# Kernel tuning notes

Hardware: AMD Instinct MI355X
Metric: run time of the kernel (lower is better)

## Reference

```python
import jax, jax.numpy as jnp
import numpy as np

NUM_NODE = 50000
NUM_EDGE = 1_600_000
NUM_REL = 512
DIM = 64


def setup_inputs() -> dict:
    key = jax.random.key(0)
    k1, k2, k3, k4, k5, k6 = jax.random.split(key, 6)
    inp = jax.random.normal(k1, (NUM_NODE, DIM), dtype=jnp.float32)
    boundary = jax.random.normal(k2, (NUM_NODE, DIM), dtype=jnp.float32)
    node_in = jax.random.randint(k3, (NUM_EDGE,), 0, NUM_NODE)
    node_out = jax.random.randint(k4, (NUM_EDGE,), 0, NUM_NODE)
    rel = jax.random.randint(k5, (NUM_EDGE,), 0, NUM_REL)
    edge_list = jnp.stack([node_in, node_out, rel], axis=1).astype(jnp.int32)
    edge_weight = jnp.ones((NUM_EDGE,), dtype=jnp.float32)
    relation_weight = jax.random.normal(k6, (NUM_REL, DIM), dtype=jnp.float32)
    W = jax.random.normal(jax.random.fold_in(key, 7), (DIM, DIM), dtype=jnp.float32) / np.sqrt(DIM)
    b = jnp.zeros((DIM,), dtype=jnp.float32)
    return {"input": inp, "boundary": boundary, "edge_list": edge_list,
            "edge_weight": edge_weight, "relation_weight": relation_weight,
            "W": W, "b": b}


def reference(input, boundary, edge_list, edge_weight, relation_weight, W, b):
    node_in = edge_list[:, 0]
    node_out = edge_list[:, 1]
    rel = edge_list[:, 2]
    # message: DistMult = x_src * r_e   [E, D]
    msg = input[node_in] * relation_weight[rel]
    msg = msg * edge_weight[:, None]
    # std aggregation: sum and sq_sum scatters, boundary acts as an extra self-message
    s = jax.ops.segment_sum(msg, node_out, num_segments=NUM_NODE) + boundary
    sq = jax.ops.segment_sum(msg * msg, node_out, num_segments=NUM_NODE) + boundary * boundary
    deg = jax.ops.segment_sum(jnp.ones_like(edge_weight), node_out, num_segments=NUM_NODE)
    deg1 = (deg + 1.0)[:, None]  # degree_out + 1 (boundary counted)
    update = jnp.sqrt(jnp.clip(sq / deg1 - (s / deg1) ** 2, 1e-6))
    # add_model: single Linear (MLP with num_mlp_layer=1, no trailing activation)
    return update @ W.T + b
```

## Files before the change

kernel.cpp:

```cpp
#include <hip/hip_runtime.h>
#include <hip/hip_bf16.h>
#include <hip/hip_fp16.h>

#define NN  50000
#define NE  1600000
#define DIM 64
#define NBK 391

#define OFF_FLAGS  0
#define OFF_BOFF   8
#define OFF_BCUR   400
#define OFF_ROWPTR 792
#define OFF_INP16  50800
#define OFF_RELW16 1650800
#define OFF_EIDX_H 1667184

#define CHUNK 2048
#define SBCAP 8192

typedef __bf16 bf16x8 __attribute__((ext_vector_type(8)));
typedef __bf16 bf16x4 __attribute__((ext_vector_type(4)));
typedef float  f32x4  __attribute__((ext_vector_type(4)));

__device__ __forceinline__ float loadF(const void* p, int i, int bf) {
  if (bf) return __bfloat162float(((const __hip_bfloat16*)p)[i]);
  return ((const float*)p)[i];
}

__device__ __forceinline__ float4 loadF4(const void* p, int i4, int bf) {
  if (bf) {
    ushort4 u = ((const ushort4*)p)[i4];
    float4 f;
    union { unsigned int ui; float fl; } c;
    c.ui = (unsigned int)u.x << 16; f.x = c.fl;
    c.ui = (unsigned int)u.y << 16; f.y = c.fl;
    c.ui = (unsigned int)u.z << 16; f.z = c.fl;
    c.ui = (unsigned int)u.w << 16; f.w = c.fl;
    return f;
  }
  return ((const float4*)p)[i4];
}

__device__ __forceinline__ float4 h4f(ushort4 u) {
  float4 f;
  f.x = __half2float(__ushort_as_half(u.x));
  f.y = __half2float(__ushort_as_half(u.y));
  f.z = __half2float(__ushort_as_half(u.z));
  f.w = __half2float(__ushort_as_half(u.w));
  return f;
}

__device__ __forceinline__ void accum(ushort4 ua, ushort4 ur,
                                      float4& s4, float4& q4) {
  float4 a = h4f(ua), r = h4f(ur);
  float tx = a.x * r.x, ty = a.y * r.y, tz = a.z * r.z, tw = a.w * r.w;
  s4.x += tx; q4.x = fmaf(tx, tx, q4.x);
  s4.y += ty; q4.y = fmaf(ty, ty, q4.y);
  s4.z += tz; q4.z = fmaf(tz, tz, q4.z);
  s4.w += tw; q4.w = fmaf(tw, tw, q4.w);
}

__global__ void k_detect(const void* input, const void* boundary,
                         const void* relw, const void* W, const void* ew,
                         int* flags, int* boff) {
  __shared__ int cnt;
  int t = threadIdx.x;
  const void* arrs[4] = {input, boundary, relw, W};
  for (int a = 0; a < 4; ++a) {
    if (t == 0) cnt = 0;
    __syncthreads();
    const unsigned short* u = (const unsigned short*)arrs[a];
    unsigned ex = (u[2 * t] >> 7) & 0xFF;
    if (ex >= 100 && ex <= 140) atomicAdd(&cnt, 1);
    __syncthreads();
    if (t == 0) flags[a] = (cnt >= 32) ? 1 : 0;
    __syncthreads();
  }
  if (t == 0) {
    flags[4] = (((const unsigned short*)ew)[0] == 0x3F80) ? 1 : 0;
    flags[5] = 1;
  }
  for (int i = t; i < 392; i += 64) boff[i] = 0;
}

__global__ __launch_bounds__(256) void k_stage(const void* __restrict__ in,
                                               const void* __restrict__ rw,
                                               unsigned short* __restrict__ inph,
                                               unsigned short* __restrict__ rwh,
                                               const int* __restrict__ flags) {
  if (flags[0] || flags[2]) return;
  int i = blockIdx.x * 256 + threadIdx.x;
  if (i < NN * 16) {
    float4 v = ((const float4*)in)[i];
    ushort4 h;
    h.x = __half_as_ushort(__float2half(v.x));
    h.y = __half_as_ushort(__float2half(v.y));
    h.z = __half_as_ushort(__float2half(v.z));
    h.w = __half_as_ushort(__float2half(v.w));
    ((ushort4*)inph)[i] = h;
  }
  if (i < 512 * 16) {
    float4 v = ((const float4*)rw)[i];
    ushort4 h;
    h.x = __half_as_ushort(__float2half(v.x));
    h.y = __half_as_ushort(__float2half(v.y));
    h.z = __half_as_ushort(__float2half(v.z));
    h.w = __half_as_ushort(__float2half(v.w));
    ((ushort4*)rwh)[i] = h;
  }
}

__global__ __launch_bounds__(256) void k_bhist(const int* __restrict__ el,
                                               const void* __restrict__ ew,
                                               int* __restrict__ bcnt,
                                               int* __restrict__ flags) {
  __shared__ int lc[NBK];
  int t = threadIdx.x;
  int bfE = flags[4];
  for (int i = t; i < NBK; i += 256) lc[i] = 0;
  __syncthreads();
  int c0 = blockIdx.x * 8192;
  int bad = 0;
  for (int i = t; i < 8192; i += 256) {
    int e = c0 + i;
    if (e < NE) {
      atomicAdd(&lc[el[e * 3 + 1] >> 7], 1);
      if (loadF(ew, e, bfE) != 1.0f) bad = 1;
    }
  }
  if (bad) flags[5] = 0;
  __syncthreads();
  for (int i = t; i < NBK; i += 256)
    if (lc[i]) atomicAdd(&bcnt[i], lc[i]);
}

__global__ __launch_bounds__(256) void k_scanb(int* __restrict__ boff,
                                               int* __restrict__ bcur,
                                               int* __restrict__ rowptr) {
  __shared__ int sc[256];
  int t = threadIdx.x;
  int i0 = 2 * t, i1 = 2 * t + 1;
  int a = (i0 < 392) ? boff[i0] : 0;
  int b = (i1 < 392) ? boff[i1] : 0;
  sc[t] = a + b;
  __syncthreads();
  for (int off = 1; off < 256; off <<= 1) {
    int v = (t >= off) ? sc[t - off] : 0;
    __syncthreads();
    sc[t] += v;
    __syncthreads();
  }
  int excl = sc[t] - (a + b);
  if (i0 < 392) boff[i0] = excl;
  if (i1 < 392) boff[i1] = excl + a;
  if (i0 < NBK) bcur[i0] = excl;
  if (i1 < NBK) bcur[i1] = excl + a;
  if (t == 255) rowptr[NN] = sc[255];
}

__global__ __launch_bounds__(256) void k_parta(
    const int* __restrict__ el, int* __restrict__ bcur,
    int* __restrict__ eidx, const int* __restrict__ flags,
    const int* __restrict__ boff, int gb0, int gb1, int cap) {
  __shared__ int stage[CHUNK];
  __shared__ unsigned short sbk[CHUNK];
  __shared__ int lh[NBK], lbase[NBK], lh2[NBK], gbs[NBK];
  __shared__ int sc[256];
  __shared__ int total;
  int t = threadIdx.x;
  int nb = gb1 - gb0;
  int c0 = blockIdx.x * CHUNK;
  int ones = flags[5];
  int base0 = boff[gb0];
  for (int i = t; i < nb; i += 256) { lh[i] = 0; lh2[i] = 0; }
  __syncthreads();
  for (int i = t; i < CHUNK; i += 256) {
    int e = c0 + i;
    if (e < NE) {
      int b = (el[e * 3 + 1] >> 7) - gb0;
      if (b >= 0 && b < nb) atomicAdd(&lh[b], 1);
    }
  }
  __syncthreads();
  int a0 = (2 * t < nb) ? lh[2 * t] : 0;
  int a1 = (2 * t + 1 < nb) ? lh[2 * t + 1] : 0;
  sc[t] = a0 + a1;
  __syncthreads();
  for (int off = 1; off < 256; off <<= 1) {
    int v = (t >= off) ? sc[t - off] : 0;
    __syncthreads();
    sc[t] += v;
    __syncthreads();
  }
  int excl = sc[t] - (a0 + a1);
  if (2 * t < nb) {
    lbase[2 * t] = excl;
    if (a0 > 0) gbs[2 * t] = atomicAdd(&bcur[gb0 + 2 * t], a0);
  }
  if (2 * t + 1 < nb) {
    lbase[2 * t + 1] = excl + a0;
    if (a1 > 0) gbs[2 * t + 1] = atomicAdd(&bcur[gb0 + 2 * t + 1], a1);
  }
  if (t == 255) total = sc[255];
  __syncthreads();
  for (int i = t; i < CHUNK; i += 256) {
    int e = c0 + i;
    if (e < NE) {
      int nout = el[e * 3 + 1];
      int b = (nout >> 7) - gb0;
      if (b >= 0 && b < nb) {
        int r = atomicAdd(&lh2[b], 1);
        int slot = lbase[b] + r;
        int rec = ones ? (el[e * 3] | (el[e * 3 + 2] << 16) |
                          ((nout & 127) << 25))
                       : (e | ((nout & 127) << 25));
        stage[slot] = rec;
        sbk[slot] = (unsigned short)b;
      }
    }
  }
  __syncthreads();
  int tot = total;
  for (int i = t; i < tot; i += 256) {
    int b = sbk[i];
    int dst = gbs[b] + (i - lbase[b]) - base0;
    if (dst >= 0 && dst < cap) eidx[dst] = stage[i];
  }
}

__global__ __launch_bounds__(256) void k_partb(
    int* __restrict__ eidx, const int* __restrict__ boff,
    int* __restrict__ rowptr, const int* __restrict__ el,
    const int* __restrict__ flags, int gb0, int cap) {
  __shared__ int ld[SBCAP];
  __shared__ int lcnt[128], lexc[128];
  int t = threadIdx.x;
  int b = gb0 + blockIdx.x;
  int n0 = b * 128;
  int ncnt = min(128, NN - n0);
  int base0 = boff[gb0];
  int rbase = boff[b], rend = boff[b + 1];
  int cnt = rend - rbase;
  int fast = (cnt <= SBCAP) && (rend - base0 <= cap);
  if (t < 128) lcnt[t] = 0;
  __syncthreads();
  if (fast) {
    for (int i = t; i < cnt; i += 256) ld[i] = eidx[rbase - base0 + i];
    __syncthreads();
    for (int i = t; i < cnt; i += 256)
      atomicAdd(&lcnt[(((unsigned)ld[i]) >> 25) & 127], 1);
  } else {
    int lim = n0 + ncnt;
    for (int e = t; e < NE; e += 256) {
      int nout = el[e * 3 + 1];
      if (nout >= n0 && nout < lim) atomicAdd(&lcnt[nout - n0], 1);
    }
  }
  __syncthreads();
  if (t < 128) lexc[t] = lcnt[t];
  __syncthreads();
  for (int off = 1; off < 128; off <<= 1) {
    int v = 0;
    if (t < 128 && t >= off) v = lexc[t - off];
    __syncthreads();
    if (t < 128) lexc[t] += v;
    __syncthreads();
  }
  if (t < 128) lexc[t] -= lcnt[t];
  __syncthreads();
  if (t < ncnt) rowptr[n0 + t] = rbase + lexc[t];
  if (t == 0) rowptr[n0 + ncnt] = rend;
  if (t < 128) lcnt[t] = 0;
  __syncthreads();
  if (fast) {
    for (int i = t; i < cnt; i += 256) {
      int rec = ld[i];
      int l = (((unsigned)rec) >> 25) & 127;
      int r = atomicAdd(&lcnt[l], 1);
      int dst = rbase + lexc[l] + r - base0;
      if (dst >= 0 && dst < cap) eidx[dst] = rec & 0x1FFFFFF;
    }
  } else {
    int ones = flags[5];
    int lim = n0 + ncnt;
    for (int e = t; e < NE; e += 256) {
      int nout = el[e * 3 + 1];
      if (nout >= n0 && nout < lim) {
        int l = nout - n0;
        int r = atomicAdd(&lcnt[l], 1);
        int dst = rbase + lexc[l] + r - base0;
        int rec = ones ? (el[e * 3] | (el[e * 3 + 2] << 16)) : e;
        if (dst >= 0 && dst < cap) eidx[dst] = rec;
      }
    }
  }
}

__global__ __launch_bounds__(256, 4) void k_node(
    const void* __restrict__ input, const void* __restrict__ boundary,
    const int* __restrict__ el, const void* __restrict__ ew,
    const void* __restrict__ relw, const void* __restrict__ W,
    const void* __restrict__ bv, const int* __restrict__ rowptr,
    const int* __restrict__ eidx, const int* __restrict__ flags,
    const unsigned short* __restrict__ inph,
    const unsigned short* __restrict__ rwh,
    void* __restrict__ out, int lo, int hi, int cap) {
  __shared__ __bf16 updb[16][72];

  int bfI = flags[0], bfB = flags[1], bfR = flags[2], bfW = flags[3],
      bfE = flags[4], ones = flags[5];
  int t  = threadIdx.x;
  int wv = t >> 6, ln = t & 63;
  int g  = ln >> 4;
  int k  = ln & 15;
  int q  = ln >> 4;
  int n0 = lo + blockIdx.x * 16;
  int base0 = rowptr[lo];

  int cc = wv * 16 + (ln & 15);
  bf16x8 bfr0, bfr1;
  #pragma unroll
  for (int j = 0; j < 8; ++j) {
    bfr0[j] = (__bf16)loadF(W, cc * 64 + q * 8 + j, bfW);
    bfr1[j] = (__bf16)loadF(W, cc * 64 + 32 + q * 8 + j, bfW);
  }
  float bias = loadF(bv, cc, bfW);

  const ushort4* ih4 = (const ushort4*)inph;
  const ushort4* rh4 = (const ushort4*)rwh;
  int hot = (!bfI && !bfR && ones) ? 1 : 0;
  int hotH = hot && (inph != 0);

  for (int rr = 0; rr < 4; ++rr) {
    int row = wv * 4 + rr;
    int n = n0 + row;
    if (n >= hi) {
      updb[row][ln] = (__bf16)0.0f;
      continue;
    }
    int start = rowptr[n] - base0, end = rowptr[n + 1] - base0;
    int deg = end - start;
    float4 s4 = {0.f,0.f,0.f,0.f}, q4 = {0.f,0.f,0.f,0.f};
    if (hotH) {
      for (int base = start; base < end; base += 64) {
        int mm = end - base; if (mm > 64) mm = 64;
        int rec = 0;
        int idx2 = base + ln;
        if (ln < mm && idx2 < cap) rec = eidx[idx2];
        int jq = mm >> 2;
        int jmax = (mm + 3) >> 2;
        int j = 0;
        for (; j + 4 <= jq; j += 4) {
          int pk0 = __shfl(rec, j * 4 + g);
          int pk1 = __shfl(rec, j * 4 + 4 + g);
          int pk2 = __shfl(rec, j * 4 + 8 + g);
          int pk3 = __shfl(rec, j * 4 + 12 + g);
          ushort4 a0 = ih4[(pk0 & 0xFFFF) * 16 + k];
          ushort4 r0 = rh4[((pk0 >> 16) & 0x1FF) * 16 + k];
          ushort4 a1 = ih4[(pk1 & 0xFFFF) * 16 + k];
          ushort4 r1 = rh4[((pk1 >> 16) & 0x1FF) * 16 + k];
          ushort4 a2 = ih4[(pk2 & 0xFFFF) * 16 + k];
          ushort4 r2 = rh4[((pk2 >> 16) & 0x1FF) * 16 + k];
          ushort4 a3 = ih4[(pk3 & 0xFFFF) * 16 + k];
          ushort4 r3 = rh4[((pk3 >> 16) & 0x1FF) * 16 + k];
          accum(a0, r0, s4, q4);
          accum(a1, r1, s4, q4);
          accum(a2, r2, s4, q4);
          accum(a3, r3, s4, q4);
        }
        for (; j < jq; ++j) {
          int pk = __shfl(rec, j * 4 + g);
          ushort4 a = ih4[(pk & 0xFFFF) * 16 + k];
          ushort4 r = rh4[((pk >> 16) & 0x1FF) * 16 + k];
          accum(a, r, s4, q4);
        }
        for (; j < jmax; ++j) {
          int slot = j * 4 + g;
          int pk = __shfl(rec, slot & 63);
          float wsel = (slot < mm) ? 1.0f : 0.0f;
          ushort4 ua = ih4[(pk & 0xFFFF) * 16 + k];
          ushort4 ur = rh4[((pk >> 16) & 0x1FF) * 16 + k];
          float4 a = h4f(ua), r = h4f(ur);
          float tx = a.x*r.x, ty = a.y*r.y, tz = a.z*r.z, tw = a.w*r.w;
          s4.x = fmaf(wsel, tx, s4.x); q4.x = fmaf(wsel*tx, tx, q4.x);
          s4.y = fmaf(wsel, ty, s4.y); q4.y = fmaf(wsel*ty, ty, q4.y);
          s4.z = fmaf(wsel, tz, s4.z); q4.z = fmaf(wsel*tz, tz, q4.z);
          s4.w = fmaf(wsel, tw, s4.w); q4.w = fmaf(wsel*tw, tw, q4.w);
        }
      }
    } else {
      for (int base = start; base < end; base += 64) {
        int mm = end - base; if (mm > 64) mm = 64;
        int rec = 0; float wrec = 0.0f;
        int idx2 = base + ln;
        if (ln < mm && idx2 < cap) {
          rec = eidx[idx2] & 0x1FFFFFF;
          if (!ones) wrec = loadF(ew, rec, bfE);
        }
        int jmax = (mm + 3) >> 2;
        for (int j = 0; j < jmax; ++j) {
          int slot = j * 4 + g;
          int rj = __shfl(rec, slot);
          int nin, rl; float wj;
          if (ones) { nin = rj & 0xFFFF; rl = (rj >> 16) & 0x1FF; wj = 1.0f; }
          else      { nin = el[rj * 3]; rl = el[rj * 3 + 2];
                      wj = __shfl(wrec, slot); }
          float wsel = (slot < mm) ? wj : 0.0f;
          float4 a = loadF4(input, nin * 16 + k, bfI);
          float4 r = loadF4(relw, rl * 16 + k, bfR);
          float tx = a.x*r.x, ty = a.y*r.y, tz = a.z*r.z, tw = a.w*r.w;
          s4.x = fmaf(wsel, tx, s4.x); q4.x = fmaf(wsel*tx, tx, q4.x);
          s4.y = fmaf(wsel, ty, s4.y); q4.y = fmaf(wsel*ty, ty, q4.y);
          s4.z = fmaf(wsel, tz, s4.z); q4.z = fmaf(wsel*tz, tz, q4.z);
          s4.w = fmaf(wsel, tw, s4.w); q4.w = fmaf(wsel*tw, tw, q4.w);
        }
      }
    }
    s4.x += __shfl_xor(s4.x, 16); s4.x += __shfl_xor(s4.x, 32);
    s4.y += __shfl_xor(s4.y, 16); s4.y += __shfl_xor(s4.y, 32);
    s4.z += __shfl_xor(s4.z, 16); s4.z += __shfl_xor(s4.z, 32);
    s4.w += __shfl_xor(s4.w, 16); s4.w += __shfl_xor(s4.w, 32);
    q4.x += __shfl_xor(q4.x, 16); q4.x += __shfl_xor(q4.x, 32);
    q4.y += __shfl_xor(q4.y, 16); q4.y += __shfl_xor(q4.y, 32);
    q4.z += __shfl_xor(q4.z, 16); q4.z += __shfl_xor(q4.z, 32);
    q4.w += __shfl_xor(q4.w, 16); q4.w += __shfl_xor(q4.w, 32);
    if (g == 0) {
      float4 b4 = loadF4(boundary, n * 16 + k, bfB);
      float dg = (float)deg + 1.0f;
      float sv, qv;
      bf16x4 u;
      sv = (s4.x + b4.x) / dg; qv = (q4.x + b4.x * b4.x) / dg;
      u[0] = (__bf16)sqrtf(fmaxf(qv - sv * sv, 1e-6f));
      sv = (s4.y + b4.y) / dg; qv = (q4.y + b4.y * b4.y) / dg;
      u[1] = (__bf16)sqrtf(fmaxf(qv - sv * sv, 1e-6f));
      sv = (s4.z + b4.z) / dg; qv = (q4.z + b4.z * b4.z) / dg;
      u[2] = (__bf16)sqrtf(fmaxf(qv - sv * sv, 1e-6f));
      sv = (s4.w + b4.w) / dg; qv = (q4.w + b4.w * b4.w) / dg;
      u[3] = (__bf16)sqrtf(fmaxf(qv - sv * sv, 1e-6f));
      *(bf16x4*)&updb[row][4 * k] = u;
    }
  }
  __syncthreads();

  bf16x8 af0 = *(const bf16x8*)&updb[ln & 15][q * 8];
  bf16x8 af1 = *(const bf16x8*)&updb[ln & 15][32 + q * 8];
  f32x4 acc = {0.f, 0.f, 0.f, 0.f};
  acc = __builtin_amdgcn_mfma_f32_16x16x32_bf16(af0, bfr0, acc, 0, 0, 0);
  acc = __builtin_amdgcn_mfma_f32_16x16x32_bf16(af1, bfr1, acc, 0, 0, 0);
  #pragma unroll
  for (int i = 0; i < 4; ++i) {
    int n = n0 + q * 4 + i;
    if (n < hi) {
      float v = acc[i] + bias;
      if (bfI) ((__hip_bfloat16*)out)[n * 64 + cc] = __float2bfloat16(v);
      else     ((float*)out)[n * 64 + cc] = v;
    }
  }
}

extern "C" void kernel_launch(void* const* d_in, const int* in_sizes, int n_in,
                              void* d_out, int out_size, void* d_ws, size_t ws_size,
                              hipStream_t stream) {
  const void* input    = d_in[0];
  const void* boundary = d_in[1];
  const int*  edges    = (const int*)d_in[2];
  const void* eweight  = d_in[3];
  const void* relw     = d_in[4];
  const void* W        = d_in[5];
  const void* bv       = d_in[6];

  int* wsI    = (int*)d_ws;
  int* flags  = wsI + OFF_FLAGS;
  int* boff   = wsI + OFF_BOFF;
  int* bcur   = wsI + OFF_BCUR;
  int* rowptr = wsI + OFF_ROWPTR;

  long avail = (long)(ws_size / 4) - OFF_INP16;
  int useH = (avail >= (long)NE + 1600000 + 16384) ? 1 : 0;
  unsigned short* inph = useH ? (unsigned short*)(wsI + OFF_INP16) : 0;
  unsigned short* rwh  = useH ? (unsigned short*)(wsI + OFF_RELW16) : 0;
  int* eidx = useH ? (wsI + OFF_EIDX_H) : (wsI + OFF_INP16);
  long cap = useH ? (avail - 1600000 - 16384) : avail;
  if (cap < 1) cap = 1;
  int npass;
  if      (cap >= (long)NE) npass = 1;
  else if (cap >= 1000000)  npass = 2;
  else if (cap >= 520000)   npass = 4;
  else                      npass = 8;

  k_detect<<<1, 64, 0, stream>>>(input, boundary, relw, W, eweight,
                                 flags, boff);
  if (useH)
    k_stage<<<(NN * 16 + 255) / 256, 256, 0, stream>>>(input, relw, inph,
                                                       rwh, flags);
  k_bhist<<<(NE + 8191) / 8192, 256, 0, stream>>>(edges, eweight, boff, flags);
  k_scanb<<<1, 256, 0, stream>>>(boff, bcur, rowptr);

  const int PA_NB = (NE + CHUNK - 1) / CHUNK;
  for (int p = 0; p < npass; ++p) {
    int gb0 = NBK * p / npass;
    int gb1 = NBK * (p + 1) / npass;
    int lo = gb0 * 128;
    int hi = (gb1 * 128 < NN) ? gb1 * 128 : NN;
    k_parta<<<PA_NB, 256, 0, stream>>>(edges, bcur, eidx, flags, boff,
                                       gb0, gb1, (int)cap);
    k_partb<<<gb1 - gb0, 256, 0, stream>>>(eidx, boff, rowptr, edges, flags,
                                           gb0, (int)cap);
    k_node<<<(hi - lo + 15) / 16, 256, 0, stream>>>(
        input, boundary, edges, eweight, relw, W, bv, rowptr, eidx, flags,
        inph, rwh, d_out, lo, hi, (int)cap);
  }
}
```

Before: 259.5 us.

## Cache relation weights in LDS with 1024-thread node blocks

k_node now runs 1024-thread blocks covering 64 nodes and copies the whole bf16 relation-weight table (64 KB) into shared memory, so the per-edge relation gathers become LDS reads instead of global loads. The updb staging buffer now reuses that shared array: the table is dead by then and results wait in registers across an extra barrier. The W fragment load is moved after aggregation and mapped per wave to a column quarter. It also doubles the edge-partition CHUNK. The 64 KB of LDS per block limits occupancy, and each block pays a table fill.

After: 251.9 us. 2.9% less time.

```diff
diff --git a/kernel.cpp b/kernel.cpp
--- a/kernel.cpp
+++ b/kernel.cpp
@@ -15,7 +15,7 @@
 #define OFF_RELW16 1650800
 #define OFF_EIDX_H 1667184
 
-#define CHUNK 2048
+#define CHUNK 4096
 #define SBCAP 8192
 
 typedef __bf16 bf16x8 __attribute__((ext_vector_type(8)));
@@ -296,7 +296,7 @@
   }
 }
 
-__global__ __launch_bounds__(256, 4) void k_node(
+__global__ __launch_bounds__(1024, 8) void k_node(
     const void* __restrict__ input, const void* __restrict__ boundary,
     const int* __restrict__ el, const void* __restrict__ ew,
     const void* __restrict__ relw, const void* __restrict__ W,
@@ -305,7 +305,8 @@
     const unsigned short* __restrict__ inph,
     const unsigned short* __restrict__ rwh,
     void* __restrict__ out, int lo, int hi, int cap) {
-  __shared__ __bf16 updb[16][72];
+  __shared__ ushort4 smraw[8192];
+  __bf16 (*updb)[72] = reinterpret_cast<__bf16(*)[72]>(smraw);
 
   int bfI = flags[0], bfB = flags[1], bfR = flags[2], bfW = flags[3],
       bfE = flags[4], ones = flags[5];
@@ -314,30 +315,30 @@
   int g  = ln >> 4;
   int k  = ln & 15;
   int q  = ln >> 4;
-  int n0 = lo + blockIdx.x * 16;
+  int n0 = lo + blockIdx.x * 64;
   int base0 = rowptr[lo];
-
-  int cc = wv * 16 + (ln & 15);
-  bf16x8 bfr0, bfr1;
-  #pragma unroll
-  for (int j = 0; j < 8; ++j) {
-    bfr0[j] = (__bf16)loadF(W, cc * 64 + q * 8 + j, bfW);
-    bfr1[j] = (__bf16)loadF(W, cc * 64 + 32 + q * 8 + j, bfW);
-  }
-  float bias = loadF(bv, cc, bfW);
+  int tt = wv >> 2, cq = wv & 3;
 
   const ushort4* ih4 = (const ushort4*)inph;
-  const ushort4* rh4 = (const ushort4*)rwh;
   int hot = (!bfI && !bfR && ones) ? 1 : 0;
   int hotH = hot && (inph != 0);
 
+  if (hotH) {
+    const ushort4* rh4g = (const ushort4*)rwh;
+    for (int i = t; i < 8192; i += 1024) smraw[i] = rh4g[i];
+  }
+  __syncthreads();
+
+  bf16x4 usv[4];
+
+  #pragma unroll
   for (int rr = 0; rr < 4; ++rr) {
     int row = wv * 4 + rr;
     int n = n0 + row;
-    if (n >= hi) {
-      updb[row][ln] = (__bf16)0.0f;
-      continue;
-    }
+    bf16x4 uz; uz[0] = (__bf16)0.f; uz[1] = (__bf16)0.f;
+    uz[2] = (__bf16)0.f; uz[3] = (__bf16)0.f;
+    usv[rr] = uz;
+    if (n >= hi) continue;
     int start = rowptr[n] - base0, end = rowptr[n + 1] - base0;
     int deg = end - start;
     float4 s4 = {0.f,0.f,0.f,0.f}, q4 = {0.f,0.f,0.f,0.f};
@@ -356,13 +357,13 @@
           int pk2 = __shfl(rec, j * 4 + 8 + g);
           int pk3 = __shfl(rec, j * 4 + 12 + g);
           ushort4 a0 = ih4[(pk0 & 0xFFFF) * 16 + k];
-          ushort4 r0 = rh4[((pk0 >> 16) & 0x1FF) * 16 + k];
           ushort4 a1 = ih4[(pk1 & 0xFFFF) * 16 + k];
-          ushort4 r1 = rh4[((pk1 >> 16) & 0x1FF) * 16 + k];
           ushort4 a2 = ih4[(pk2 & 0xFFFF) * 16 + k];
-          ushort4 r2 = rh4[((pk2 >> 16) & 0x1FF) * 16 + k];
           ushort4 a3 = ih4[(pk3 & 0xFFFF) * 16 + k];
-          ushort4 r3 = rh4[((pk3 >> 16) & 0x1FF) * 16 + k];
+          ushort4 r0 = smraw[((pk0 >> 16) & 0x1FF) * 16 + k];
+          ushort4 r1 = smraw[((pk1 >> 16) & 0x1FF) * 16 + k];
+          ushort4 r2 = smraw[((pk2 >> 16) & 0x1FF) * 16 + k];
+          ushort4 r3 = smraw[((pk3 >> 16) & 0x1FF) * 16 + k];
           accum(a0, r0, s4, q4);
           accum(a1, r1, s4, q4);
           accum(a2, r2, s4, q4);
@@ -371,7 +372,7 @@
         for (; j < jq; ++j) {
           int pk = __shfl(rec, j * 4 + g);
           ushort4 a = ih4[(pk & 0xFFFF) * 16 + k];
-          ushort4 r = rh4[((pk >> 16) & 0x1FF) * 16 + k];
+          ushort4 r = smraw[((pk >> 16) & 0x1FF) * 16 + k];
           accum(a, r, s4, q4);
         }
         for (; j < jmax; ++j) {
@@ -379,7 +380,7 @@
           int pk = __shfl(rec, slot & 63);
           float wsel = (slot < mm) ? 1.0f : 0.0f;
           ushort4 ua = ih4[(pk & 0xFFFF) * 16 + k];
-          ushort4 ur = rh4[((pk >> 16) & 0x1FF) * 16 + k];
+          ushort4 ur = smraw[((pk >> 16) & 0x1FF) * 16 + k];
           float4 a = h4f(ua), r = h4f(ur);
           float tx = a.x*r.x, ty = a.y*r.y, tz = a.z*r.z, tw = a.w*r.w;
           s4.x = fmaf(wsel, tx, s4.x); q4.x = fmaf(wsel*tx, tx, q4.x);
@@ -437,19 +438,34 @@
       u[2] = (__bf16)sqrtf(fmaxf(qv - sv * sv, 1e-6f));
       sv = (s4.w + b4.w) / dg; qv = (q4.w + b4.w * b4.w) / dg;
       u[3] = (__bf16)sqrtf(fmaxf(qv - sv * sv, 1e-6f));
-      *(bf16x4*)&updb[row][4 * k] = u;
-    }
-  }
-  __syncthreads();
-
-  bf16x8 af0 = *(const bf16x8*)&updb[ln & 15][q * 8];
-  bf16x8 af1 = *(const bf16x8*)&updb[ln & 15][32 + q * 8];
+      usv[rr] = u;
+    }
+  }
+  __syncthreads();
+  if (g == 0) {
+    #pragma unroll
+    for (int rr = 0; rr < 4; ++rr)
+      *(bf16x4*)&updb[wv * 4 + rr][4 * k] = usv[rr];
+  }
+  __syncthreads();
+
+  int cc = cq * 16 + (ln & 15);
+  bf16x8 bfr0, bfr1;
+  #pragma unroll
+  for (int j = 0; j < 8; ++j) {
+    bfr0[j] = (__bf16)loadF(W, cc * 64 + q * 8 + j, bfW);
+    bfr1[j] = (__bf16)loadF(W, cc * 64 + 32 + q * 8 + j, bfW);
+  }
+  float bias = loadF(bv, cc, bfW);
+
+  bf16x8 af0 = *(const bf16x8*)&updb[tt * 16 + (ln & 15)][q * 8];
+  bf16x8 af1 = *(const bf16x8*)&updb[tt * 16 + (ln & 15)][32 + q * 8];
   f32x4 acc = {0.f, 0.f, 0.f, 0.f};
   acc = __builtin_amdgcn_mfma_f32_16x16x32_bf16(af0, bfr0, acc, 0, 0, 0);
   acc = __builtin_amdgcn_mfma_f32_16x16x32_bf16(af1, bfr1, acc, 0, 0, 0);
   #pragma unroll
   for (int i = 0; i < 4; ++i) {
-    int n = n0 + q * 4 + i;
+    int n = n0 + tt * 16 + q * 4 + i;
     if (n < hi) {
       float v = acc[i] + bias;
       if (bfI) ((__hip_bfloat16*)out)[n * 64 + cc] = __float2bfloat16(v);
@@ -506,7 +522,7 @@
                                        gb0, gb1, (int)cap);
     k_partb<<<gb1 - gb0, 256, 0, stream>>>(eidx, boff, rowptr, edges, flags,
                                            gb0, (int)cap);
-    k_node<<<(hi - lo + 15) / 16, 256, 0, stream>>>(
+    k_node<<<(hi - lo + 63) / 64, 1024, 0, stream>>>(
         input, boundary, edges, eweight, relw, W, bv, rowptr, eidx, flags,
         inph, rwh, d_out, lo, hi, (int)cap);
   }
```

## Fuse per-bucket local sort into node kernel, keep sorted edges in LDS

Applied to the files above, without the earlier changes.

Merges the bucket-local counting sort (k_partb) into the node aggregation kernel. Each 1024-thread block now owns one 128-node bucket, sorts its edges into shared memory and reads them from LDS instead of writing and re-reading a global CSR (rowptr). This removes one kernel launch and a global round trip of the edge index array. The slow fallback becomes a per-node full edge scan, and occupancy drops to 391 blocks of 1024 threads, which lowers parallelism per pass. CHUNK in the partition kernel is also doubled.

Result: faster. 241.1 us (-7.1%).

```diff
diff --git a/kernel.cpp b/kernel.cpp
--- a/kernel.cpp
+++ b/kernel.cpp
@@ -10,13 +10,12 @@
 #define OFF_FLAGS  0
 #define OFF_BOFF   8
 #define OFF_BCUR   400
-#define OFF_ROWPTR 792
 #define OFF_INP16  50800
 #define OFF_RELW16 1650800
 #define OFF_EIDX_H 1667184
 
-#define CHUNK 2048
-#define SBCAP 8192
+#define CHUNK 4096
+#define SBCAP 7936
 
 typedef __bf16 bf16x8 __attribute__((ext_vector_type(8)));
 typedef __bf16 bf16x4 __attribute__((ext_vector_type(4)));
@@ -135,8 +134,7 @@
 }
 
 __global__ __launch_bounds__(256) void k_scanb(int* __restrict__ boff,
-                                               int* __restrict__ bcur,
-                                               int* __restrict__ rowptr) {
+                                               int* __restrict__ bcur) {
   __shared__ int sc[256];
   int t = threadIdx.x;
   int i0 = 2 * t, i1 = 2 * t + 1;
@@ -155,7 +153,6 @@
   if (i1 < 392) boff[i1] = excl + a;
   if (i0 < NBK) bcur[i0] = excl;
   if (i1 < NBK) bcur[i1] = excl + a;
-  if (t == 255) rowptr[NN] = sc[255];
 }
 
 __global__ __launch_bounds__(256) void k_parta(
@@ -228,193 +225,173 @@
   }
 }
 
-__global__ __launch_bounds__(256) void k_partb(
-    int* __restrict__ eidx, const int* __restrict__ boff,
-    int* __restrict__ rowptr, const int* __restrict__ el,
-    const int* __restrict__ flags, int gb0, int cap) {
+__global__ __launch_bounds__(1024, 8) void k_node(
+    const void* __restrict__ input, const void* __restrict__ boundary,
+    const int* __restrict__ el, const void* __restrict__ ew,
+    const void* __restrict__ relw, const void* __restrict__ W,
+    const void* __restrict__ bv, const int* __restrict__ boff,
+    const int* __restrict__ eidx, const int* __restrict__ flags,
+    const unsigned short* __restrict__ inph,
+    const unsigned short* __restrict__ rwh,
+    void* __restrict__ out, int gb0, int hi, int cap) {
   __shared__ int ld[SBCAP];
-  __shared__ int lcnt[128], lexc[128];
+  __shared__ int ld2[SBCAP];
+  __shared__ int lstart[128], lend[128], lcnt[128];
+  __bf16 (*updb)[72] = reinterpret_cast<__bf16(*)[72]>(ld);
+
+  int bfI = flags[0], bfB = flags[1], bfR = flags[2], bfW = flags[3],
+      bfE = flags[4], ones = flags[5];
   int t = threadIdx.x;
-  int b = gb0 + blockIdx.x;
-  int n0 = b * 128;
-  int ncnt = min(128, NN - n0);
+  int wv = t >> 6, ln = t & 63;
+  int g = ln >> 4;
+  int k = ln & 15;
+  int q = ln >> 4;
+  int B = gb0 + blockIdx.x;
+  int n0 = B * 128;
   int base0 = boff[gb0];
-  int rbase = boff[b], rend = boff[b + 1];
+  int rbase = boff[B], rend = boff[B + 1];
   int cnt = rend - rbase;
   int fast = (cnt <= SBCAP) && (rend - base0 <= cap);
+
   if (t < 128) lcnt[t] = 0;
   __syncthreads();
   if (fast) {
-    for (int i = t; i < cnt; i += 256) ld[i] = eidx[rbase - base0 + i];
-    __syncthreads();
-    for (int i = t; i < cnt; i += 256)
+    for (int i = t; i < cnt; i += 1024) ld[i] = eidx[rbase - base0 + i];
+    __syncthreads();
+    for (int i = t; i < cnt; i += 1024)
       atomicAdd(&lcnt[(((unsigned)ld[i]) >> 25) & 127], 1);
-  } else {
-    int lim = n0 + ncnt;
-    for (int e = t; e < NE; e += 256) {
-      int nout = el[e * 3 + 1];
-      if (nout >= n0 && nout < lim) atomicAdd(&lcnt[nout - n0], 1);
-    }
-  }
-  __syncthreads();
-  if (t < 128) lexc[t] = lcnt[t];
+  }
+  __syncthreads();
+  if (t < 128) lend[t] = lcnt[t];
   __syncthreads();
   for (int off = 1; off < 128; off <<= 1) {
     int v = 0;
-    if (t < 128 && t >= off) v = lexc[t - off];
-    __syncthreads();
-    if (t < 128) lexc[t] += v;
-    __syncthreads();
-  }
-  if (t < 128) lexc[t] -= lcnt[t];
-  __syncthreads();
-  if (t < ncnt) rowptr[n0 + t] = rbase + lexc[t];
-  if (t == 0) rowptr[n0 + ncnt] = rend;
-  if (t < 128) lcnt[t] = 0;
+    if (t < 128 && t >= off) v = lend[t - off];
+    __syncthreads();
+    if (t < 128) lend[t] += v;
+    __syncthreads();
+  }
+  if (t < 128) { lstart[t] = lend[t] - lcnt[t]; lcnt[t] = 0; }
   __syncthreads();
   if (fast) {
-    for (int i = t; i < cnt; i += 256) {
+    for (int i = t; i < cnt; i += 1024) {
       int rec = ld[i];
       int l = (((unsigned)rec) >> 25) & 127;
       int r = atomicAdd(&lcnt[l], 1);
-      int dst = rbase + lexc[l] + r - base0;
-      if (dst >= 0 && dst < cap) eidx[dst] = rec & 0x1FFFFFF;
-    }
-  } else {
-    int ones = flags[5];
-    int lim = n0 + ncnt;
-    for (int e = t; e < NE; e += 256) {
-      int nout = el[e * 3 + 1];
-      if (nout >= n0 && nout < lim) {
-        int l = nout - n0;
-        int r = atomicAdd(&lcnt[l], 1);
-        int dst = rbase + lexc[l] + r - base0;
-        int rec = ones ? (el[e * 3] | (el[e * 3 + 2] << 16)) : e;
-        if (dst >= 0 && dst < cap) eidx[dst] = rec;
-      }
-    }
-  }
-}
-
-__global__ __launch_bounds__(256, 4) void k_node(
-    const void* __restrict__ input, const void* __restrict__ boundary,
-    const int* __restrict__ el, const void* __restrict__ ew,
-    const void* __restrict__ relw, const void* __restrict__ W,
-    const void* __restrict__ bv, const int* __restrict__ rowptr,
-    const int* __restrict__ eidx, const int* __restrict__ flags,
-    const unsigned short* __restrict__ inph,
-    const unsigned short* __restrict__ rwh,
-    void* __restrict__ out, int lo, int hi, int cap) {
-  __shared__ __bf16 updb[16][72];
-
-  int bfI = flags[0], bfB = flags[1], bfR = flags[2], bfW = flags[3],
-      bfE = flags[4], ones = flags[5];
-  int t  = threadIdx.x;
-  int wv = t >> 6, ln = t & 63;
-  int g  = ln >> 4;
-  int k  = ln & 15;
-  int q  = ln >> 4;
-  int n0 = lo + blockIdx.x * 16;
-  int base0 = rowptr[lo];
-
-  int cc = wv * 16 + (ln & 15);
-  bf16x8 bfr0, bfr1;
-  #pragma unroll
-  for (int j = 0; j < 8; ++j) {
-    bfr0[j] = (__bf16)loadF(W, cc * 64 + q * 8 + j, bfW);
-    bfr1[j] = (__bf16)loadF(W, cc * 64 + 32 + q * 8 + j, bfW);
-  }
-  float bias = loadF(bv, cc, bfW);
+      ld2[lstart[l] + r] = rec;
+    }
+  }
+  __syncthreads();
 
   const ushort4* ih4 = (const ushort4*)inph;
   const ushort4* rh4 = (const ushort4*)rwh;
-  int hot = (!bfI && !bfR && ones) ? 1 : 0;
-  int hotH = hot && (inph != 0);
-
-  for (int rr = 0; rr < 4; ++rr) {
-    int row = wv * 4 + rr;
+  int hot = (!bfI && !bfR && ones && inph != 0) ? 1 : 0;
+
+  for (int rr = 0; rr < 8; ++rr) {
+    int row = wv * 8 + rr;
     int n = n0 + row;
     if (n >= hi) {
-      updb[row][ln] = (__bf16)0.0f;
+      if (g == 0) *(bf16x4*)&updb[row][4 * k] =
+          bf16x4{(__bf16)0.f, (__bf16)0.f, (__bf16)0.f, (__bf16)0.f};
       continue;
     }
-    int start = rowptr[n] - base0, end = rowptr[n + 1] - base0;
-    int deg = end - start;
     float4 s4 = {0.f,0.f,0.f,0.f}, q4 = {0.f,0.f,0.f,0.f};
-    if (hotH) {
-      for (int base = start; base < end; base += 64) {
-        int mm = end - base; if (mm > 64) mm = 64;
-        int rec = 0;
-        int idx2 = base + ln;
-        if (ln < mm && idx2 < cap) rec = eidx[idx2];
-        int jq = mm >> 2;
-        int jmax = (mm + 3) >> 2;
-        int j = 0;
-        for (; j + 4 <= jq; j += 4) {
-          int pk0 = __shfl(rec, j * 4 + g);
-          int pk1 = __shfl(rec, j * 4 + 4 + g);
-          int pk2 = __shfl(rec, j * 4 + 8 + g);
-          int pk3 = __shfl(rec, j * 4 + 12 + g);
-          ushort4 a0 = ih4[(pk0 & 0xFFFF) * 16 + k];
-          ushort4 r0 = rh4[((pk0 >> 16) & 0x1FF) * 16 + k];
-          ushort4 a1 = ih4[(pk1 & 0xFFFF) * 16 + k];
-          ushort4 r1 = rh4[((pk1 >> 16) & 0x1FF) * 16 + k];
-          ushort4 a2 = ih4[(pk2 & 0xFFFF) * 16 + k];
-          ushort4 r2 = rh4[((pk2 >> 16) & 0x1FF) * 16 + k];
-          ushort4 a3 = ih4[(pk3 & 0xFFFF) * 16 + k];
-          ushort4 r3 = rh4[((pk3 >> 16) & 0x1FF) * 16 + k];
-          accum(a0, r0, s4, q4);
-          accum(a1, r1, s4, q4);
-          accum(a2, r2, s4, q4);
-          accum(a3, r3, s4, q4);
+    float degf = 0.f;
+    if (fast) {
+      int start = lstart[row], end = lend[row];
+      degf = (float)(end - start);
+      if (hot) {
+        for (int base = start; base < end; base += 64) {
+          int mm = end - base; if (mm > 64) mm = 64;
+          int rec = 0;
+          if (ln < mm) rec = ld2[base + ln];
+          int jq = mm >> 2;
+          int jmax = (mm + 3) >> 2;
+          int j = 0;
+          for (; j + 4 <= jq; j += 4) {
+            int pk0 = __shfl(rec, j * 4 + g);
+            int pk1 = __shfl(rec, j * 4 + 4 + g);
+            int pk2 = __shfl(rec, j * 4 + 8 + g);
+            int pk3 = __shfl(rec, j * 4 + 12 + g);
+            ushort4 a0 = ih4[(pk0 & 0xFFFF) * 16 + k];
+            ushort4 r0 = rh4[((pk0 >> 16) & 0x1FF) * 16 + k];
+            ushort4 a1 = ih4[(pk1 & 0xFFFF) * 16 + k];
+            ushort4 r1 = rh4[((pk1 >> 16) & 0x1FF) * 16 + k];
+            ushort4 a2 = ih4[(pk2 & 0xFFFF) * 16 + k];
+            ushort4 r2 = rh4[((pk2 >> 16) & 0x1FF) * 16 + k];
+            ushort4 a3 = ih4[(pk3 & 0xFFFF) * 16 + k];
+            ushort4 r3 = rh4[((pk3 >> 16) & 0x1FF) * 16 + k];
+            accum(a0, r0, s4, q4);
+            accum(a1, r1, s4, q4);
+            accum(a2, r2, s4, q4);
+            accum(a3, r3, s4, q4);
+          }
+          for (; j < jq; ++j) {
+            int pk = __shfl(rec, j * 4 + g);
+            ushort4 a = ih4[(pk & 0xFFFF) * 16 + k];
+            ushort4 r = rh4[((pk >> 16) & 0x1FF) * 16 + k];
+            accum(a, r, s4, q4);
+          }
+          for (; j < jmax; ++j) {
+            int slot = j * 4 + g;
+            int pk = __shfl(rec, slot & 63);
+            float wsel = (slot < mm) ? 1.0f : 0.0f;
+            ushort4 ua = ih4[(pk & 0xFFFF) * 16 + k];
+            ushort4 ur = rh4[((pk >> 16) & 0x1FF) * 16 + k];
+            float4 a = h4f(ua), r = h4f(ur);
+            float tx = a.x*r.x, ty = a.y*r.y, tz = a.z*r.z, tw = a.w*r.w;
+            s4.x = fmaf(wsel, tx, s4.x); q4.x = fmaf(wsel*tx, tx, q4.x);
+            s4.y = fmaf(wsel, ty, s4.y); q4.y = fmaf(wsel*ty, ty, q4.y);
+            s4.z = fmaf(wsel, tz, s4.z); q4.z = fmaf(wsel*tz, tz, q4.z);
+            s4.w = fmaf(wsel, tw, s4.w); q4.w = fmaf(wsel*tw, tw, q4.w);
+          }
         }
-        for (; j < jq; ++j) {
-          int pk = __shfl(rec, j * 4 + g);
-          ushort4 a = ih4[(pk & 0xFFFF) * 16 + k];
-          ushort4 r = rh4[((pk >> 16) & 0x1FF) * 16 + k];
-          accum(a, r, s4, q4);
-        }
-        for (; j < jmax; ++j) {
-          int slot = j * 4 + g;
-          int pk = __shfl(rec, slot & 63);
-          float wsel = (slot < mm) ? 1.0f : 0.0f;
-          ushort4 ua = ih4[(pk & 0xFFFF) * 16 + k];
-          ushort4 ur = rh4[((pk >> 16) & 0x1FF) * 16 + k];
-          float4 a = h4f(ua), r = h4f(ur);
-          float tx = a.x*r.x, ty = a.y*r.y, tz = a.z*r.z, tw = a.w*r.w;
-          s4.x = fmaf(wsel, tx, s4.x); q4.x = fmaf(wsel*tx, tx, q4.x);
-          s4.y = fmaf(wsel, ty, s4.y); q4.y = fmaf(wsel*ty, ty, q4.y);
-          s4.z = fmaf(wsel, tz, s4.z); q4.z = fmaf(wsel*tz, tz, q4.z);
-          s4.w = fmaf(wsel, tw, s4.w); q4.w = fmaf(wsel*tw, tw, q4.w);
+      } else {
+        for (int base = start; base < end; base += 64) {
+          int mm = end - base; if (mm > 64) mm = 64;
+          int rec = 0; float wrec = 0.0f;
+          if (ln < mm) {
+            rec = ld2[base + ln] & 0x1FFFFFF;
+            if (!ones) wrec = loadF(ew, rec, bfE);
+          }
+          int jmax = (mm + 3) >> 2;
+          for (int j = 0; j < jmax; ++j) {
+            int slot = j * 4 + g;
+            int rj = __shfl(rec, slot);
+            int nin, rl; float wj;
+            if (ones) { nin = rj & 0xFFFF; rl = (rj >> 16) & 0x1FF; wj = 1.0f; }
+            else      { nin = el[rj * 3]; rl = el[rj * 3 + 2];
+                        wj = __shfl(wrec, slot); }
+            float wsel = (slot < mm) ? wj : 0.0f;
+            float4 a = loadF4(input, nin * 16 + k, bfI);
+            float4 r = loadF4(relw, rl * 16 + k, bfR);
+            float tx = a.x*r.x, ty = a.y*r.y, tz = a.z*r.z, tw = a.w*r.w;
+            s4.x = fmaf(wsel, tx, s4.x); q4.x = fmaf(wsel*tx, tx, q4.x);
+            s4.y = fmaf(wsel, ty, s4.y); q4.y = fmaf(wsel*ty, ty, q4.y);
+            s4.z = fmaf(wsel, tz, s4.z); q4.z = fmaf(wsel*tz, tz, q4.z);
+            s4.w = fmaf(wsel, tw, s4.w); q4.w = fmaf(wsel*tw, tw, q4.w);
+          }
         }
       }
     } else {
-      for (int base = start; base < end; base += 64) {
-        int mm = end - base; if (mm > 64) mm = 64;
-        int rec = 0; float wrec = 0.0f;
-        int idx2 = base + ln;
-        if (ln < mm && idx2 < cap) {
-          rec = eidx[idx2] & 0x1FFFFFF;
-          if (!ones) wrec = loadF(ew, rec, bfE);
-        }
-        int jmax = (mm + 3) >> 2;
-        for (int j = 0; j < jmax; ++j) {
-          int slot = j * 4 + g;
-          int rj = __shfl(rec, slot);
-          int nin, rl; float wj;
-          if (ones) { nin = rj & 0xFFFF; rl = (rj >> 16) & 0x1FF; wj = 1.0f; }
-          else      { nin = el[rj * 3]; rl = el[rj * 3 + 2];
-                      wj = __shfl(wrec, slot); }
-          float wsel = (slot < mm) ? wj : 0.0f;
-          float4 a = loadF4(input, nin * 16 + k, bfI);
-          float4 r = loadF4(relw, rl * 16 + k, bfR);
-          float tx = a.x*r.x, ty = a.y*r.y, tz = a.z*r.z, tw = a.w*r.w;
-          s4.x = fmaf(wsel, tx, s4.x); q4.x = fmaf(wsel*tx, tx, q4.x);
-          s4.y = fmaf(wsel, ty, s4.y); q4.y = fmaf(wsel*ty, ty, q4.y);
-          s4.z = fmaf(wsel, tz, s4.z); q4.z = fmaf(wsel*tz, tz, q4.z);
-          s4.w = fmaf(wsel, tw, s4.w); q4.w = fmaf(wsel*tw, tw, q4.w);
-        }
+      float degc = 0.f;
+      for (int e0 = g; e0 < NE; e0 += 4) {
+        int nout = el[e0 * 3 + 1];
+        if (nout != n) continue;
+        degc += 1.0f;
+        int nin = el[e0 * 3], rl = el[e0 * 3 + 2];
+        float wj = ones ? 1.0f : loadF(ew, e0, bfE);
+        float4 a = loadF4(input, nin * 16 + k, bfI);
+        float4 r = loadF4(relw, rl * 16 + k, bfR);
+        float tx = wj*a.x*r.x, ty = wj*a.y*r.y, tz = wj*a.z*r.z,
+              tw = wj*a.w*r.w;
+        s4.x += tx; q4.x = fmaf(tx, tx, q4.x);
+        s4.y += ty; q4.y = fmaf(ty, ty, q4.y);
+        s4.z += tz; q4.z = fmaf(tz, tz, q4.z);
+        s4.w += tw; q4.w = fmaf(tw, tw, q4.w);
       }
+      degc += __shfl_xor(degc, 16); degc += __shfl_xor(degc, 32);
+      degf = degc;
     }
     s4.x += __shfl_xor(s4.x, 16); s4.x += __shfl_xor(s4.x, 32);
     s4.y += __shfl_xor(s4.y, 16); s4.y += __shfl_xor(s4.y, 32);
@@ -426,7 +403,7 @@
     q4.w += __shfl_xor(q4.w, 16); q4.w += __shfl_xor(q4.w, 32);
     if (g == 0) {
       float4 b4 = loadF4(boundary, n * 16 + k, bfB);
-      float dg = (float)deg + 1.0f;
+      float dg = degf + 1.0f;
       float sv, qv;
       bf16x4 u;
       sv = (s4.x + b4.x) / dg; qv = (q4.x + b4.x * b4.x) / dg;
@@ -442,18 +419,30 @@
   }
   __syncthreads();
 
-  bf16x8 af0 = *(const bf16x8*)&updb[ln & 15][q * 8];
-  bf16x8 af1 = *(const bf16x8*)&updb[ln & 15][32 + q * 8];
-  f32x4 acc = {0.f, 0.f, 0.f, 0.f};
-  acc = __builtin_amdgcn_mfma_f32_16x16x32_bf16(af0, bfr0, acc, 0, 0, 0);
-  acc = __builtin_amdgcn_mfma_f32_16x16x32_bf16(af1, bfr1, acc, 0, 0, 0);
+  int tt = wv >> 1, chh = wv & 1;
+  bf16x8 af0 = *(const bf16x8*)&updb[tt * 16 + (ln & 15)][q * 8];
+  bf16x8 af1 = *(const bf16x8*)&updb[tt * 16 + (ln & 15)][32 + q * 8];
   #pragma unroll
-  for (int i = 0; i < 4; ++i) {
-    int n = n0 + q * 4 + i;
-    if (n < hi) {
-      float v = acc[i] + bias;
-      if (bfI) ((__hip_bfloat16*)out)[n * 64 + cc] = __float2bfloat16(v);
-      else     ((float*)out)[n * 64 + cc] = v;
+  for (int hh = 0; hh < 2; ++hh) {
+    int cc = chh * 32 + hh * 16 + (ln & 15);
+    bf16x8 bfr0, bfr1;
+    #pragma unroll
+    for (int j = 0; j < 8; ++j) {
+      bfr0[j] = (__bf16)loadF(W, cc * 64 + q * 8 + j, bfW);
+      bfr1[j] = (__bf16)loadF(W, cc * 64 + 32 + q * 8 + j, bfW);
+    }
+    float bias = loadF(bv, cc, bfW);
+    f32x4 accv = {0.f, 0.f, 0.f, 0.f};
+    accv = __builtin_amdgcn_mfma_f32_16x16x32_bf16(af0, bfr0, accv, 0, 0, 0);
+    accv = __builtin_amdgcn_mfma_f32_16x16x32_bf16(af1, bfr1, accv, 0, 0, 0);
+    #pragma unroll
+    for (int i = 0; i < 4; ++i) {
+      int nn = n0 + tt * 16 + q * 4 + i;
+      if (nn < hi) {
+        float v = accv[i] + bias;
+        if (bfI) ((__hip_bfloat16*)out)[nn * 64 + cc] = __float2bfloat16(v);
+        else     ((float*)out)[nn * 64 + cc] = v;
+      }
     }
   }
 }
@@ -473,7 +462,6 @@
   int* flags  = wsI + OFF_FLAGS;
   int* boff   = wsI + OFF_BOFF;
   int* bcur   = wsI + OFF_BCUR;
-  int* rowptr = wsI + OFF_ROWPTR;
 
   long avail = (long)(ws_size / 4) - OFF_INP16;
   int useH = (avail >= (long)NE + 1600000 + 16384) ? 1 : 0;
@@ -494,20 +482,17 @@
     k_stage<<<(NN * 16 + 255) / 256, 256, 0, stream>>>(input, relw, inph,
                                                        rwh, flags);
   k_bhist<<<(NE + 8191) / 8192, 256, 0, stream>>>(edges, eweight, boff, flags);
-  k_scanb<<<1, 256, 0, stream>>>(boff, bcur, rowptr);
+  k_scanb<<<1, 256, 0, stream>>>(boff, bcur);
 
   const int PA_NB = (NE + CHUNK - 1) / CHUNK;
   for (int p = 0; p < npass; ++p) {
     int gb0 = NBK * p / npass;
     int gb1 = NBK * (p + 1) / npass;
-    int lo = gb0 * 128;
     int hi = (gb1 * 128 < NN) ? gb1 * 128 : NN;
     k_parta<<<PA_NB, 256, 0, stream>>>(edges, bcur, eidx, flags, boff,
                                        gb0, gb1, (int)cap);
-    k_partb<<<gb1 - gb0, 256, 0, stream>>>(eidx, boff, rowptr, edges, flags,
-                                           gb0, (int)cap);
-    k_node<<<(hi - lo + 15) / 16, 256, 0, stream>>>(
-        input, boundary, edges, eweight, relw, W, bv, rowptr, eidx, flags,
-        inph, rwh, d_out, lo, hi, (int)cap);
-  }
-}
+    k_node<<<gb1 - gb0, 1024, 0, stream>>>(
+        input, boundary, edges, eweight, relw, W, bv, boff, eidx, flags,
+        inph, rwh, d_out, gb0, hi, (int)cap);
+  }
+}
```
